# Kernel tuning notes

Hardware: AMD Instinct MI355X
Metric: run time of the kernel (lower is better)

## Reference

```python
import jax, jax.numpy as jnp
import numpy as np

DIM = 1024
DIM_HEAD = 64
HEADS = 16
INNER = DIM_HEAD * HEADS  # 1024
EPS = 1e-5


def layernorm(x, g, b):
    mu = jnp.mean(x, axis=-1, keepdims=True)
    var = jnp.var(x, axis=-1, keepdims=True)
    return (x - mu) * jax.lax.rsqrt(var + EPS) * g + b


def setup_inputs() -> dict:
    key = jax.random.key(0)
    ks = jax.random.split(key, 8)
    b, n_media, n_lat = 16, 4096, 64
    x = jax.random.normal(ks[0], (b, n_media, DIM), dtype=jnp.float32)
    latents = jax.random.normal(ks[1], (b, n_lat, DIM), dtype=jnp.float32)
    s = 0.02
    Wq = jax.random.normal(ks[2], (DIM, INNER), dtype=jnp.float32) * s
    Wkv = jax.random.normal(ks[3], (DIM, 2 * INNER), dtype=jnp.float32) * s
    Wout = jax.random.normal(ks[4], (INNER, DIM), dtype=jnp.float32) * s
    return {
        "x": x,
        "latents": latents,
        "g_media": jnp.ones((DIM,), jnp.float32),
        "b_media": jnp.zeros((DIM,), jnp.float32),
        "g_lat": jnp.ones((DIM,), jnp.float32),
        "b_lat": jnp.zeros((DIM,), jnp.float32),
        "Wq": Wq,
        "Wkv": Wkv,
        "Wout": Wout,
    }


def reference(x, latents, g_media, b_media, g_lat, b_lat, Wq, Wkv, Wout):
    h, d = HEADS, DIM_HEAD
    scale = d ** -0.5
    x = layernorm(x, g_media, b_media)
    latents = layernorm(latents, g_lat, b_lat)
    q = latents @ Wq                                  # [b, i, inner]
    kv_input = jnp.concatenate([x, latents], axis=1)  # [b, j, dim]
    kv = kv_input @ Wkv                               # [b, j, 2*inner]
    k, v = jnp.split(kv, 2, axis=-1)
    B = q.shape[0]
    q = q.reshape(B, -1, h, d).transpose(0, 2, 1, 3) * scale  # [b, h, i, d]
    k = k.reshape(B, -1, h, d).transpose(0, 2, 1, 3)          # [b, h, j, d]
    v = v.reshape(B, -1, h, d).transpose(0, 2, 1, 3)
    sim = jnp.einsum('bhid,bhjd->bhij', q, k)
    attn = jax.nn.softmax(sim, axis=-1)  # max-subtract handled internally
    out = jnp.einsum('bhij,bhjd->bhid', attn, v)
    out = out.transpose(0, 2, 1, 3).reshape(B, -1, h * d)
    return out @ Wout
```

## Files before the change

kernel.cpp:

```cpp
#include <hip/hip_runtime.h>
#include <cstdint>
#include <cstddef>

typedef short bf16x8 __attribute__((ext_vector_type(8)));
typedef float floatx4 __attribute__((ext_vector_type(4)));

__device__ __forceinline__ float b2f(short s) {
  union { float f; unsigned u; } v; v.u = ((unsigned)(unsigned short)s) << 16; return v.f;
}
__device__ __forceinline__ short f2b(float f) {
  union { float f; unsigned u; } v; v.f = f;
  unsigned r = v.u + 0x7fffu + ((v.u >> 16) & 1u);
  return (short)(r >> 16);
}

__device__ __forceinline__ void gld_lds16(const void* g, void* l) {
  __builtin_amdgcn_global_load_lds((const __attribute__((address_space(1))) void*)g,
                                   (__attribute__((address_space(3))) void*)l, 16, 0, 0);
}

__device__ __forceinline__ void row_load16(const void* p, size_t eoff, bool isf, float* f) {
  if (isf) {
    const float4* r4 = (const float4*)((const float*)p + eoff);
    float4 a = r4[0], b = r4[1], c = r4[2], d = r4[3];
    f[0] = a.x; f[1] = a.y; f[2] = a.z; f[3] = a.w;
    f[4] = b.x; f[5] = b.y; f[6] = b.z; f[7] = b.w;
    f[8] = c.x; f[9] = c.y; f[10] = c.z; f[11] = c.w;
    f[12] = d.x; f[13] = d.y; f[14] = d.z; f[15] = d.w;
  } else {
    const short* rp = (const short*)p + eoff;
    bf16x8 v0 = *(const bf16x8*)rp, v1 = *(const bf16x8*)(rp + 8);
    const short* s0 = (const short*)&v0;
    const short* s1 = (const short*)&v1;
#pragma unroll
    for (int e = 0; e < 8; ++e) { f[e] = b2f(s0[e]); f[8 + e] = b2f(s1[e]); }
  }
}

__device__ __forceinline__ bool inputs_are_f32(const unsigned* sent) {
  return sent[0] != 0x3F803F80u;
}

__global__ __launch_bounds__(256) void ln_x_kernel(const void* __restrict__ x,
    const void* __restrict__ g, const void* __restrict__ b,
    short* __restrict__ lnkv, const unsigned* __restrict__ sent) {
  bool isf = inputs_are_f32(sent);
  int lane = threadIdx.x & 63, wv = threadIdx.x >> 6;
  int row = blockIdx.x * 4 + wv;
  float f[16], gg[16], bb[16];
  row_load16(x, (size_t)row * 1024 + lane * 16, isf, f);
  float sum = 0.f, sq = 0.f;
#pragma unroll
  for (int e = 0; e < 16; ++e) { sum += f[e]; sq += f[e] * f[e]; }
#pragma unroll
  for (int m = 1; m <= 32; m <<= 1) { sum += __shfl_xor(sum, m); sq += __shfl_xor(sq, m); }
  float mean = sum * (1.f / 1024.f);
  float var = sq * (1.f / 1024.f) - mean * mean;
  float rstd = rsqrtf(var + 1e-5f);
  row_load16(g, (size_t)lane * 16, isf, gg);
  row_load16(b, (size_t)lane * 16, isf, bb);
  bf16x8 o0, o1; short* os0 = (short*)&o0; short* os1 = (short*)&o1;
#pragma unroll
  for (int e = 0; e < 8; ++e) {
    os0[e] = f2b((f[e] - mean) * rstd * gg[e] + bb[e]);
    os1[e] = f2b((f[8 + e] - mean) * rstd * gg[8 + e] + bb[8 + e]);
  }
  size_t orow = (size_t)(row >> 12) * 4160 + (row & 4095);
  short* op = lnkv + orow * 1024 + lane * 16;
  *(bf16x8*)op = o0; *(bf16x8*)(op + 8) = o1;
}

__global__ __launch_bounds__(256) void ln_lat_kernel(const void* __restrict__ lat,
    const void* __restrict__ g, const void* __restrict__ b,
    short* __restrict__ lnlat, short* __restrict__ lnkv,
    const unsigned* __restrict__ sent) {
  bool isf = inputs_are_f32(sent);
  int lane = threadIdx.x & 63, wv = threadIdx.x >> 6;
  int row = blockIdx.x * 4 + wv;
  float f[16], gg[16], bb[16];
  row_load16(lat, (size_t)row * 1024 + lane * 16, isf, f);
  float sum = 0.f, sq = 0.f;
#pragma unroll
  for (int e = 0; e < 16; ++e) { sum += f[e]; sq += f[e] * f[e]; }
#pragma unroll
  for (int m = 1; m <= 32; m <<= 1) { sum += __shfl_xor(sum, m); sq += __shfl_xor(sq, m); }
  float mean = sum * (1.f / 1024.f);
  float var = sq * (1.f / 1024.f) - mean * mean;
  float rstd = rsqrtf(var + 1e-5f);
  row_load16(g, (size_t)lane * 16, isf, gg);
  row_load16(b, (size_t)lane * 16, isf, bb);
  bf16x8 o0, o1; short* os0 = (short*)&o0; short* os1 = (short*)&o1;
#pragma unroll
  for (int e = 0; e < 8; ++e) {
    os0[e] = f2b((f[e] - mean) * rstd * gg[e] + bb[e]);
    os1[e] = f2b((f[8 + e] - mean) * rstd * gg[8 + e] + bb[8 + e]);
  }
  short* op1 = lnlat + (size_t)row * 1024 + lane * 16;
  *(bf16x8*)op1 = o0; *(bf16x8*)(op1 + 8) = o1;
  size_t orow = (size_t)(row >> 6) * 4160 + 4096 + (row & 63);
  short* op2 = lnkv + orow * 1024 + lane * 16;
  *(bf16x8*)op2 = o0; *(bf16x8*)(op2 + 8) = o1;
}

__global__ __launch_bounds__(256) void transpose_any(const void* __restrict__ in,
    short* __restrict__ out, int R, int C, const unsigned* __restrict__ sent) {
  bool isf = inputs_are_f32(sent);
  __shared__ short tile[32][33];
  int tx = threadIdx.x & 31, ty = threadIdx.x >> 5;
  int c0 = blockIdx.x * 32, r0 = blockIdx.y * 32;
#pragma unroll
  for (int i = 0; i < 32; i += 8) {
    size_t idx = (size_t)(r0 + ty + i) * C + c0 + tx;
    tile[ty + i][tx] = isf ? f2b(((const float*)in)[idx]) : ((const short*)in)[idx];
  }
  __syncthreads();
#pragma unroll
  for (int i = 0; i < 32; i += 8)
    out[(size_t)(c0 + ty + i) * R + r0 + tx] = tile[tx][ty + i];
}

__global__ __launch_bounds__(256) void gemm_bt(const short* __restrict__ A,
    const short* __restrict__ Bt, short* __restrict__ Cb, float* __restrict__ Cf,
    int M, int N, int K) {
  __shared__ short As[128][32];
  __shared__ short Bs[128][32];
  int tid = threadIdx.x;
  int wave = tid >> 6, lane = tid & 63;
  int quad = lane >> 4, l15 = lane & 15;
  int wm = (wave >> 1) * 64, wn = (wave & 1) * 64;
  size_t tm = (size_t)blockIdx.y * 128, tn = (size_t)blockIdx.x * 128;

  int srow = wave * 32 + (lane >> 2);
  int skoff = (((lane & 3) ^ ((lane >> 3) & 3)) * 8);
  const short* ga0 = A + (tm + srow) * (size_t)K + skoff;
  const short* ga1 = ga0 + (size_t)16 * K;
  const short* gb0 = Bt + (tn + srow) * (size_t)K + skoff;
  const short* gb1 = gb0 + (size_t)16 * K;
  char* la0 = (char*)(&As[0][0]) + (wave * 32) * 64;
  char* la1 = la0 + 16 * 64;
  char* lb0 = (char*)(&Bs[0][0]) + (wave * 32) * 64;
  char* lb1 = lb0 + 16 * 64;

  int swzr = ((l15 >> 1) & 3) * 16;

  floatx4 acc[4][4];
#pragma unroll
  for (int i = 0; i < 4; ++i)
#pragma unroll
    for (int j = 0; j < 4; ++j) acc[i][j] = (floatx4){0.f, 0.f, 0.f, 0.f};

  for (int k0 = 0; k0 < K; k0 += 32) {
    gld_lds16(ga0 + k0, la0);
    gld_lds16(ga1 + k0, la1);
    gld_lds16(gb0 + k0, lb0);
    gld_lds16(gb1 + k0, lb1);
    __syncthreads();
    bf16x8 af[4], bfv[4];
#pragma unroll
    for (int i = 0; i < 4; ++i)
      af[i] = *(const bf16x8*)((const char*)As + (wm + i * 16 + l15) * 64 + ((quad * 16) ^ swzr));
#pragma unroll
    for (int j = 0; j < 4; ++j)
      bfv[j] = *(const bf16x8*)((const char*)Bs + (wn + j * 16 + l15) * 64 + ((quad * 16) ^ swzr));
#pragma unroll
    for (int i = 0; i < 4; ++i)
#pragma unroll
      for (int j = 0; j < 4; ++j)
        acc[i][j] = __builtin_amdgcn_mfma_f32_16x16x32_bf16(af[i], bfv[j], acc[i][j], 0, 0, 0);
    __syncthreads();
  }

  if (Cf) {
#pragma unroll
    for (int i = 0; i < 4; ++i)
#pragma unroll
      for (int j = 0; j < 4; ++j)
#pragma unroll
        for (int r = 0; r < 4; ++r) {
          size_t m = tm + wm + i * 16 + quad * 4 + r;
          size_t n = tn + wn + j * 16 + l15;
          Cf[m * (size_t)N + n] = acc[i][j][r];
        }
  } else {
#pragma unroll
    for (int i = 0; i < 4; ++i)
#pragma unroll
      for (int j = 0; j < 4; ++j)
#pragma unroll
        for (int r = 0; r < 4; ++r) {
          size_t m = tm + wm + i * 16 + quad * 4 + r;
          size_t n = tn + wn + j * 16 + l15;
          Cb[m * (size_t)N + n] = f2b(acc[i][j][r]);
        }
  }
}

__global__ __launch_bounds__(512, 2) void gemm256_8ph(const short* __restrict__ A,
    const short* __restrict__ Bt, short* __restrict__ Cb, int M, int N, int K) {
  __shared__ char lds[2][65536];
  const int NT = K >> 6;

  int tid = threadIdx.x;
  int w = tid >> 6, lane = tid & 63;
  int wr = w >> 2, wc = w & 3;
  int quad = lane >> 4, l15 = lane & 15;

  int ncol = N >> 8;
  int nwg = gridDim.x * gridDim.y;
  int L = blockIdx.y * gridDim.x + blockIdx.x;
  int cpx = nwg >> 3;
  int bb = (L & 7) * cpx + (L >> 3);
  int rowp = bb / ncol;
  int col = bb - rowp * ncol;
  size_t tm = (size_t)rowp * 256, tn = (size_t)col * 256;

  int srow = tid >> 2;
  int sc8 = (((tid & 3) ^ ((srow >> 1) & 3)) << 3);
  const short* gA = A + (tm + srow) * (size_t)K + sc8;
  const short* gB = Bt + (tn + srow) * (size_t)K + sc8;
  size_t rstep = (size_t)128 * K;
  char* dA = &lds[0][0] + (size_t)w * 1024;
  char* dB = &lds[0][32768] + (size_t)w * 1024;

  auto stageA = [&](int c, int tt, int kk) {
    int ko = (tt << 6) + (kk << 5);
    char* d = dA + (size_t)c * 65536 + kk * 16384;
    gld_lds16(gA + ko, d);
    gld_lds16(gA + ko + rstep, d + 8192);
  };
  auto stageB = [&](int c, int tt, int kk) {
    int ko = (tt << 6) + (kk << 5);
    char* d = dB + (size_t)c * 65536 + kk * 16384;
    gld_lds16(gB + ko, d);
    gld_lds16(gB + ko + rstep, d + 8192);
  };

  const char* Lb = (const char*)&lds[0][0];
  int colb = ((quad ^ ((l15 >> 1) & 3)) << 4);
  auto rdA = [&](int c, int mi, int kk) -> bf16x8 {
    return *(const bf16x8*)(Lb + (size_t)c * 65536 + kk * 16384 +
                            ((wr * 128 + mi * 16 + l15) << 6) + colb);
  };
  auto rdB = [&](int c, int nj, int kk) -> bf16x8 {
    return *(const bf16x8*)(Lb + (size_t)c * 65536 + 32768 + kk * 16384 +
                            ((wc * 64 + nj * 16 + l15) << 6) + colb);
  };

  floatx4 acc[8][4];
#pragma unroll
  for (int i = 0; i < 8; ++i)
#pragma unroll
    for (int j = 0; j < 4; ++j) acc[i][j] = (floatx4){0.f, 0.f, 0.f, 0.f};

  stageA(0, 0, 0); stageA(0, 0, 1);
  stageB(0, 0, 0); stageB(0, 0, 1);
  asm volatile("s_waitcnt vmcnt(0)" ::: "memory");
  __builtin_amdgcn_s_barrier();
  asm volatile("" ::: "memory");

  for (int t = 0; t < NT; ++t) {
    int c = t & 1;
    bool st = (t + 1 < NT);
    bf16x8 afl[4][2], afh[4][2], bv[2][2];

#pragma unroll
    for (int i = 0; i < 4; ++i) { afl[i][0] = rdA(c, i, 0); afl[i][1] = rdA(c, i, 1); }
#pragma unroll
    for (int j = 0; j < 2; ++j) { bv[j][0] = rdB(c, j, 0); bv[j][1] = rdB(c, j, 1); }
    if (st) stageA(c ^ 1, t + 1, 0);
    asm volatile("" ::: "memory");
    __builtin_amdgcn_s_barrier();
    asm volatile("s_waitcnt lgkmcnt(0)" ::: "memory");
    __builtin_amdgcn_s_setprio(1);
#pragma unroll
    for (int i = 0; i < 4; ++i)
#pragma unroll
      for (int j = 0; j < 2; ++j) {
        acc[i][j] = __builtin_amdgcn_mfma_f32_16x16x32_bf16(afl[i][0], bv[j][0], acc[i][j], 0, 0, 0);
        acc[i][j] = __builtin_amdgcn_mfma_f32_16x16x32_bf16(afl[i][1], bv[j][1], acc[i][j], 0, 0, 0);
      }
    __builtin_amdgcn_s_setprio(0);
    asm volatile("" ::: "memory");
    __builtin_amdgcn_s_barrier();
    asm volatile("" ::: "memory");

#pragma unroll
    for (int i = 0; i < 4; ++i) { afh[i][0] = rdA(c, 4 + i, 0); afh[i][1] = rdA(c, 4 + i, 1); }
    if (st) stageA(c ^ 1, t + 1, 1);
    asm volatile("" ::: "memory");
    __builtin_amdgcn_s_barrier();
    asm volatile("s_waitcnt lgkmcnt(0)" ::: "memory");
    __builtin_amdgcn_s_setprio(1);
#pragma unroll
    for (int i = 0; i < 4; ++i)
#pragma unroll
      for (int j = 0; j < 2; ++j) {
        acc[4 + i][j] = __builtin_amdgcn_mfma_f32_16x16x32_bf16(afh[i][0], bv[j][0], acc[4 + i][j], 0, 0, 0);
        acc[4 + i][j] = __builtin_amdgcn_mfma_f32_16x16x32_bf16(afh[i][1], bv[j][1], acc[4 + i][j], 0, 0, 0);
      }
    __builtin_amdgcn_s_setprio(0);
    asm volatile("" ::: "memory");
    __builtin_amdgcn_s_barrier();
    asm volatile("" ::: "memory");

#pragma unroll
    for (int j = 0; j < 2; ++j) { bv[j][0] = rdB(c, 2 + j, 0); bv[j][1] = rdB(c, 2 + j, 1); }
    if (st) { stageB(c ^ 1, t + 1, 0); stageB(c ^ 1, t + 1, 1); }
    asm volatile("" ::: "memory");
    __builtin_amdgcn_s_barrier();
    asm volatile("s_waitcnt lgkmcnt(0)" ::: "memory");
    __builtin_amdgcn_s_setprio(1);
#pragma unroll
    for (int i = 0; i < 4; ++i)
#pragma unroll
      for (int j = 0; j < 2; ++j) {
        acc[4 + i][2 + j] = __builtin_amdgcn_mfma_f32_16x16x32_bf16(afh[i][0], bv[j][0], acc[4 + i][2 + j], 0, 0, 0);
        acc[4 + i][2 + j] = __builtin_amdgcn_mfma_f32_16x16x32_bf16(afh[i][1], bv[j][1], acc[4 + i][2 + j], 0, 0, 0);
      }
    __builtin_amdgcn_s_setprio(0);
    asm volatile("" ::: "memory");
    __builtin_amdgcn_s_barrier();
    asm volatile("" ::: "memory");

    __builtin_amdgcn_s_setprio(1);
#pragma unroll
    for (int i = 0; i < 4; ++i)
#pragma unroll
      for (int j = 0; j < 2; ++j) {
        acc[i][2 + j] = __builtin_amdgcn_mfma_f32_16x16x32_bf16(afl[i][0], bv[j][0], acc[i][2 + j], 0, 0, 0);
        acc[i][2 + j] = __builtin_amdgcn_mfma_f32_16x16x32_bf16(afl[i][1], bv[j][1], acc[i][2 + j], 0, 0, 0);
      }
    __builtin_amdgcn_s_setprio(0);
    if (st) asm volatile("s_waitcnt vmcnt(0)" ::: "memory");
    asm volatile("" ::: "memory");
    __builtin_amdgcn_s_barrier();
    asm volatile("" ::: "memory");
  }

  size_t crow = tm + (size_t)wr * 128 + quad * 4;
  size_t ccol = tn + (size_t)wc * 64 + l15;
#pragma unroll
  for (int i = 0; i < 8; ++i)
#pragma unroll
    for (int j = 0; j < 4; ++j)
#pragma unroll
      for (int r = 0; r < 4; ++r)
        Cb[(crow + i * 16 + r) * (size_t)N + ccol + j * 16] = f2b(acc[i][j][r]);
}

__global__ __launch_bounds__(256) void attn_kernel(const short* __restrict__ q,
    const short* __restrict__ kv, float* __restrict__ po,
    float* __restrict__ pm, float* __restrict__ pl) {
  __shared__ short Vt[64][32];
  __shared__ short Pl[4][16][32];

  int blk = blockIdx.x;
  int bh = blk >> 2, js = blk & 3;
  int b = bh >> 4, h = bh & 15;
  int tid = threadIdx.x;
  int w = tid >> 6, lane = tid & 63;
  int quad = lane >> 4, l15 = lane & 15;

  const short* qp = q + (size_t)(b * 64) * 1024 + h * 64;
  const short* kp = kv + (size_t)b * 4160 * 2048 + h * 64;
  const short* vp = kp + 1024;

  bf16x8 aq[2];
#pragma unroll
  for (int kh = 0; kh < 2; ++kh)
    aq[kh] = *(const bf16x8*)(qp + (size_t)(w * 16 + l15) * 1024 + kh * 32 + quad * 8);

  floatx4 o[4];
#pragma unroll
  for (int dt = 0; dt < 4; ++dt) o[dt] = (floatx4){0.f, 0.f, 0.f, 0.f};
  float mrun[4], lrun[4];
#pragma unroll
  for (int r = 0; r < 4; ++r) { mrun[r] = -1e30f; lrun[r] = 0.f; }

  const float scale = 0.125f;

  int vj = tid & 31;
  int vd0 = (tid >> 5) * 8;

  for (int t = js; t < 130; t += 4) {
    int j0 = t * 32;
    bf16x8 vv = *(const bf16x8*)(vp + (size_t)(j0 + vj) * 2048 + vd0);
    bf16x8 bk[2][2];
#pragma unroll
    for (int nt = 0; nt < 2; ++nt)
#pragma unroll
      for (int kh = 0; kh < 2; ++kh)
        bk[nt][kh] = *(const bf16x8*)(kp + (size_t)(j0 + nt * 16 + l15) * 2048 + kh * 32 + quad * 8);

    floatx4 z = (floatx4){0.f, 0.f, 0.f, 0.f};
    floatx4 s[2];
#pragma unroll
    for (int nt = 0; nt < 2; ++nt) {
      floatx4 a0 = __builtin_amdgcn_mfma_f32_16x16x32_bf16(aq[0], bk[nt][0], z, 0, 0, 0);
      s[nt] = __builtin_amdgcn_mfma_f32_16x16x32_bf16(aq[1], bk[nt][1], a0, 0, 0, 0);
    }

    {
      const short* vs = (const short*)&vv;
#pragma unroll
      for (int e = 0; e < 8; ++e) Vt[vd0 + e][vj] = vs[e];
    }

    float alpha[4];
#pragma unroll
    for (int r = 0; r < 4; ++r) {
      float v0 = s[0][r] * scale;
      float v1 = s[1][r] * scale;
      float tmx = fmaxf(v0, v1);
      tmx = fmaxf(tmx, __shfl_xor(tmx, 1));
      tmx = fmaxf(tmx, __shfl_xor(tmx, 2));
      tmx = fmaxf(tmx, __shfl_xor(tmx, 4));
      tmx = fmaxf(tmx, __shfl_xor(tmx, 8));
      float mn = fmaxf(mrun[r], tmx);
      float al = __expf(mrun[r] - mn);
      float p0 = __expf(v0 - mn);
      float p1 = __expf(v1 - mn);
      float ts = p0 + p1;
      ts += __shfl_xor(ts, 1);
      ts += __shfl_xor(ts, 2);
      ts += __shfl_xor(ts, 4);
      ts += __shfl_xor(ts, 8);
      lrun[r] = lrun[r] * al + ts;
      mrun[r] = mn;
      alpha[r] = al;
      int prow = quad * 4 + r;
      Pl[w][prow][l15] = f2b(p0);
      Pl[w][prow][16 + l15] = f2b(p1);
    }

#pragma unroll
    for (int dt = 0; dt < 4; ++dt)
#pragma unroll
      for (int r = 0; r < 4; ++r) o[dt][r] *= alpha[r];

    __syncthreads();

    bf16x8 aP = *(const bf16x8*)(&Pl[w][l15][0] + quad * 8);
    bf16x8 bV[4];
#pragma unroll
    for (int dt = 0; dt < 4; ++dt)
      bV[dt] = *(const bf16x8*)(&Vt[dt * 16 + l15][0] + quad * 8);
#pragma unroll
    for (int dt = 0; dt < 4; ++dt)
      o[dt] = __builtin_amdgcn_mfma_f32_16x16x32_bf16(aP, bV[dt], o[dt], 0, 0, 0);

    __syncthreads();
  }

  float* pob = po + (size_t)blk * 4096;
#pragma unroll
  for (int dt = 0; dt < 4; ++dt)
#pragma unroll
    for (int r = 0; r < 4; ++r)
      pob[(w * 16 + quad * 4 + r) * 64 + dt * 16 + l15] = o[dt][r];
  if (l15 == 0) {
#pragma unroll
    for (int r = 0; r < 4; ++r) {
      pm[(size_t)blk * 64 + w * 16 + quad * 4 + r] = mrun[r];
      pl[(size_t)blk * 64 + w * 16 + quad * 4 + r] = lrun[r];
    }
  }
}

__global__ __launch_bounds__(256) void attn_combine(const float* __restrict__ po,
    const float* __restrict__ pm, const float* __restrict__ pl,
    short* __restrict__ ao) {
  int bh = blockIdx.x;
  int b = bh >> 4, h = bh & 15;
  int tid = threadIdx.x;
  int i = tid >> 2;
  int cg = (tid & 3) * 16;
  size_t p0 = (size_t)bh * 4;
  float m0 = pm[(p0 + 0) * 64 + i], m1 = pm[(p0 + 1) * 64 + i];
  float m2 = pm[(p0 + 2) * 64 + i], m3 = pm[(p0 + 3) * 64 + i];
  float M = fmaxf(fmaxf(m0, m1), fmaxf(m2, m3));
  float w0 = __expf(m0 - M), w1 = __expf(m1 - M);
  float w2 = __expf(m2 - M), w3 = __expf(m3 - M);
  float den = pl[(p0 + 0) * 64 + i] * w0 + pl[(p0 + 1) * 64 + i] * w1 +
              pl[(p0 + 2) * 64 + i] * w2 + pl[(p0 + 3) * 64 + i] * w3;
  float rden = 1.f / den;
  const float* r0 = po + (p0 + 0) * 4096 + i * 64 + cg;
  const float* r1 = po + (p0 + 1) * 4096 + i * 64 + cg;
  const float* r2 = po + (p0 + 2) * 4096 + i * 64 + cg;
  const float* r3 = po + (p0 + 3) * 4096 + i * 64 + cg;
  short* op = ao + (size_t)(b * 64 + i) * 1024 + h * 64 + cg;
#pragma unroll
  for (int d = 0; d < 16; ++d) {
    float num = r0[d] * w0 + r1[d] * w1 + r2[d] * w2 + r3[d] * w3;
    op[d] = f2b(num * rden);
  }
}

extern "C" void kernel_launch(void* const* d_in, const int* in_sizes, int n_in,
                              void* d_out, int out_size, void* d_ws, size_t ws_size,
                              hipStream_t stream) {
  const void* x    = d_in[0];
  const void* lat  = d_in[1];
  const void* gm   = d_in[2];
  const void* bm   = d_in[3];
  const void* gl   = d_in[4];
  const void* bl   = d_in[5];
  const void* Wq   = d_in[6];
  const void* Wkv  = d_in[7];
  const void* Wout = d_in[8];
  const unsigned* sent = (const unsigned*)gm;

  char* ws = (char*)d_ws;
  size_t off = 0;
  auto alloc = [&](size_t bytes) { char* p = ws + off; off += (bytes + 255) & ~(size_t)255; return p; };
  short* kvb   = (short*)alloc((size_t)66560 * 2048 * 2);
  short* lnkv  = (short*)alloc((size_t)66560 * 1024 * 2);
  short* lnlat = (short*)alloc((size_t)1024 * 1024 * 2);
  short* qb    = (short*)alloc((size_t)1024 * 1024 * 2);
  short* ao    = (short*)alloc((size_t)1024 * 1024 * 2);
  short* WqT   = (short*)alloc((size_t)1024 * 1024 * 2);
  short* WkvT  = (short*)alloc((size_t)2048 * 1024 * 2);
  short* WoutT = (short*)alloc((size_t)1024 * 1024 * 2);
  float* po    = (float*)alloc((size_t)1024 * 4096 * 4);
  float* pm    = (float*)alloc((size_t)1024 * 64 * 4);
  float* pl    = (float*)alloc((size_t)1024 * 64 * 4);
  (void)in_sizes; (void)n_in; (void)out_size;

  if (off > ws_size) return;

  transpose_any<<<dim3(32, 32), 256, 0, stream>>>(Wq, WqT, 1024, 1024, sent);
  transpose_any<<<dim3(64, 32), 256, 0, stream>>>(Wkv, WkvT, 1024, 2048, sent);
  transpose_any<<<dim3(32, 32), 256, 0, stream>>>(Wout, WoutT, 1024, 1024, sent);
  ln_x_kernel<<<16384, 256, 0, stream>>>(x, gm, bm, lnkv, sent);
  ln_lat_kernel<<<256, 256, 0, stream>>>(lat, gl, bl, lnlat, lnkv, sent);
  gemm_bt<<<dim3(8, 8), 256, 0, stream>>>(lnlat, WqT, qb, nullptr, 1024, 1024, 1024);
  gemm256_8ph<<<dim3(8, 260), 512, 0, stream>>>(lnkv, WkvT, kvb, 66560, 2048, 1024);
  attn_kernel<<<1024, 256, 0, stream>>>(qb, kvb, po, pm, pl);
  attn_combine<<<256, 256, 0, stream>>>(po, pm, pl, ao);
  gemm_bt<<<dim3(8, 8), 256, 0, stream>>>(ao, WoutT, nullptr, (float*)d_out, 1024, 1024, 1024);
}
```

Before: 869.6 us.

## Split GEMM K-tile into two half-phases with partial vmcnt waits for deeper prefetch

Reorganizes the GEMM main loop so each K-tile is processed as two k-halves. Each half reads A and B fragments for one kk slice and issues prefetch of the matching next-tile half. Partial `s_waitcnt vmcnt(4)` replaces full drains, so the second half of the next tile's loads can stay in flight while the first half is consumed. This is meant to overlap global→LDS transfers with MFMA work and cut stall time at barriers. It relies on correct vmcnt accounting; the final-iteration wait of vmcnt(4) with no outstanding loads is harmless, but miscounting could cause races.

```diff
diff --git a/kernel.cpp b/kernel.cpp
--- a/kernel.cpp
+++ b/kernel.cpp
@@ -252,21 +252,20 @@
 #pragma unroll
     for (int j = 0; j < 4; ++j) acc[i][j] = (floatx4){0.f, 0.f, 0.f, 0.f};
 
-  stageA(0, 0, 0); stageA(0, 0, 1);
-  stageB(0, 0, 0); stageB(0, 0, 1);
-  asm volatile("s_waitcnt vmcnt(0)" ::: "memory");
+  stageA(0, 0, 0); stageB(0, 0, 0); stageA(0, 0, 1); stageB(0, 0, 1);
+  asm volatile("s_waitcnt vmcnt(4)" ::: "memory");
   __builtin_amdgcn_s_barrier();
   asm volatile("" ::: "memory");
 
   for (int t = 0; t < NT; ++t) {
     int c = t & 1;
     bool st = (t + 1 < NT);
-    bf16x8 afl[4][2], afh[4][2], bv[2][2];
-
-#pragma unroll
-    for (int i = 0; i < 4; ++i) { afl[i][0] = rdA(c, i, 0); afl[i][1] = rdA(c, i, 1); }
-#pragma unroll
-    for (int j = 0; j < 2; ++j) { bv[j][0] = rdB(c, j, 0); bv[j][1] = rdB(c, j, 1); }
+    bf16x8 afl[4], afh[4], bv[4];
+
+#pragma unroll
+    for (int i = 0; i < 4; ++i) afl[i] = rdA(c, i, 0);
+#pragma unroll
+    for (int j = 0; j < 4; ++j) bv[j] = rdB(c, j, 0);
     if (st) stageA(c ^ 1, t + 1, 0);
     asm volatile("" ::: "memory");
     __builtin_amdgcn_s_barrier();
@@ -275,18 +274,16 @@
 #pragma unroll
     for (int i = 0; i < 4; ++i)
 #pragma unroll
-      for (int j = 0; j < 2; ++j) {
-        acc[i][j] = __builtin_amdgcn_mfma_f32_16x16x32_bf16(afl[i][0], bv[j][0], acc[i][j], 0, 0, 0);
-        acc[i][j] = __builtin_amdgcn_mfma_f32_16x16x32_bf16(afl[i][1], bv[j][1], acc[i][j], 0, 0, 0);
-      }
+      for (int j = 0; j < 4; ++j)
+        acc[i][j] = __builtin_amdgcn_mfma_f32_16x16x32_bf16(afl[i], bv[j], acc[i][j], 0, 0, 0);
     __builtin_amdgcn_s_setprio(0);
     asm volatile("" ::: "memory");
     __builtin_amdgcn_s_barrier();
     asm volatile("" ::: "memory");
 
 #pragma unroll
-    for (int i = 0; i < 4; ++i) { afh[i][0] = rdA(c, 4 + i, 0); afh[i][1] = rdA(c, 4 + i, 1); }
-    if (st) stageA(c ^ 1, t + 1, 1);
+    for (int i = 0; i < 4; ++i) afh[i] = rdA(c, 4 + i, 0);
+    if (st) stageB(c ^ 1, t + 1, 0);
     asm volatile("" ::: "memory");
     __builtin_amdgcn_s_barrier();
     asm volatile("s_waitcnt lgkmcnt(0)" ::: "memory");
@@ -294,18 +291,19 @@
 #pragma unroll
     for (int i = 0; i < 4; ++i)
 #pragma unroll
-      for (int j = 0; j < 2; ++j) {
-        acc[4 + i][j] = __builtin_amdgcn_mfma_f32_16x16x32_bf16(afh[i][0], bv[j][0], acc[4 + i][j], 0, 0, 0);
-        acc[4 + i][j] = __builtin_amdgcn_mfma_f32_16x16x32_bf16(afh[i][1], bv[j][1], acc[4 + i][j], 0, 0, 0);
-      }
+      for (int j = 0; j < 4; ++j)
+        acc[4 + i][j] = __builtin_amdgcn_mfma_f32_16x16x32_bf16(afh[i], bv[j], acc[4 + i][j], 0, 0, 0);
     __builtin_amdgcn_s_setprio(0);
-    asm volatile("" ::: "memory");
-    __builtin_amdgcn_s_barrier();
-    asm volatile("" ::: "memory");
-
-#pragma unroll
-    for (int j = 0; j < 2; ++j) { bv[j][0] = rdB(c, 2 + j, 0); bv[j][1] = rdB(c, 2 + j, 1); }
-    if (st) { stageB(c ^ 1, t + 1, 0); stageB(c ^ 1, t + 1, 1); }
+    if (st) asm volatile("s_waitcnt vmcnt(4)" ::: "memory");
+    else    asm volatile("s_waitcnt vmcnt(0)" ::: "memory");
+    __builtin_amdgcn_s_barrier();
+    asm volatile("" ::: "memory");
+
+#pragma unroll
+    for (int i = 0; i < 4; ++i) afl[i] = rdA(c, i, 1);
+#pragma unroll
+    for (int j = 0; j < 4; ++j) bv[j] = rdB(c, j, 1);
+    if (st) stageA(c ^ 1, t + 1, 1);
     asm volatile("" ::: "memory");
     __builtin_amdgcn_s_barrier();
     asm volatile("s_waitcnt lgkmcnt(0)" ::: "memory");
@@ -313,26 +311,27 @@
 #pragma unroll
     for (int i = 0; i < 4; ++i)
 #pragma unroll
-      for (int j = 0; j < 2; ++j) {
-        acc[4 + i][2 + j] = __builtin_amdgcn_mfma_f32_16x16x32_bf16(afh[i][0], bv[j][0], acc[4 + i][2 + j], 0, 0, 0);
-        acc[4 + i][2 + j] = __builtin_amdgcn_mfma_f32_16x16x32_bf16(afh[i][1], bv[j][1], acc[4 + i][2 + j], 0, 0, 0);
-      }
+      for (int j = 0; j < 4; ++j)
+        acc[i][j] = __builtin_amdgcn_mfma_f32_16x16x32_bf16(afl[i], bv[j], acc[i][j], 0, 0, 0);
     __builtin_amdgcn_s_setprio(0);
     asm volatile("" ::: "memory");
     __builtin_amdgcn_s_barrier();
     asm volatile("" ::: "memory");
 
+#pragma unroll
+    for (int i = 0; i < 4; ++i) afh[i] = rdA(c, 4 + i, 1);
+    if (st) stageB(c ^ 1, t + 1, 1);
+    asm volatile("" ::: "memory");
+    __builtin_amdgcn_s_barrier();
+    asm volatile("s_waitcnt lgkmcnt(0)" ::: "memory");
     __builtin_amdgcn_s_setprio(1);
 #pragma unroll
     for (int i = 0; i < 4; ++i)
 #pragma unroll
-      for (int j = 0; j < 2; ++j) {
-        acc[i][2 + j] = __builtin_amdgcn_mfma_f32_16x16x32_bf16(afl[i][0], bv[j][0], acc[i][2 + j], 0, 0, 0);
-        acc[i][2 + j] = __builtin_amdgcn_mfma_f32_16x16x32_bf16(afl[i][1], bv[j][1], acc[i][2 + j], 0, 0, 0);
-      }
+      for (int j = 0; j < 4; ++j)
+        acc[4 + i][j] = __builtin_amdgcn_mfma_f32_16x16x32_bf16(afh[i], bv[j], acc[4 + i][j], 0, 0, 0);
     __builtin_amdgcn_s_setprio(0);
-    if (st) asm volatile("s_waitcnt vmcnt(0)" ::: "memory");
-    asm volatile("" ::: "memory");
+    asm volatile("s_waitcnt vmcnt(4)" ::: "memory");
     __builtin_amdgcn_s_barrier();
     asm volatile("" ::: "memory");
   }
```

Measured after the change: 859.2 us. Within noise of the previous version (-1.2%).
